# Kernel tuning notes

Hardware: AMD Instinct MI355X
Metric: run time of the kernel (lower is better)

Reference implementation:

```python
import jax, jax.numpy as jnp
import numpy as np

N = 50000      # nodes
E = 600000     # edges
C = 128        # in_channels
H = 128        # hidden_channels
O = 128        # out_channels
G = 512        # graphs in batch
BN_EPS = 1e-5


def setup_inputs() -> dict:
    key = jax.random.key(0)
    ks = jax.random.split(key, 16)

    def w(k, shape):
        return jax.random.normal(k, shape, dtype=jnp.float32) * 0.05

    inp = {}
    inp["x"] = jax.random.normal(ks[0], (N, C), dtype=jnp.float32)
    inp["edge_index"] = jax.random.randint(ks[1], (2, E), 0, N, dtype=jnp.int64)
    inp["batch"] = jnp.sort(jax.random.randint(ks[2], (N,), 0, G, dtype=jnp.int64))

    dims = [(C, H, H), (H, H, H), (H, H, O)]
    ki = 3
    for li, (din, dh, dout) in enumerate(dims, 1):
        inp[f"g{li}_W1"] = w(ks[ki], (din, dh)); inp[f"g{li}_b1"] = jnp.zeros((dh,), jnp.float32)
        inp[f"g{li}_gm"] = jnp.ones((dh,), jnp.float32); inp[f"g{li}_bt"] = jnp.zeros((dh,), jnp.float32)
        inp[f"g{li}_rm"] = jnp.zeros((dh,), jnp.float32); inp[f"g{li}_rv"] = jnp.ones((dh,), jnp.float32)
        inp[f"g{li}_W2"] = w(ks[ki + 1], (dh, dout)); inp[f"g{li}_b2"] = jnp.zeros((dout,), jnp.float32)
        ki += 2
    inp["lin_W"] = w(ks[ki], (H + H + O, O))
    inp["lin_b"] = jnp.zeros((O,), jnp.float32)
    return inp


def gin_conv(x, src, dst, W1, b1, gm, bt, rm, rv, W2, b2):
    # GINConv (eps=0): mlp(x + sum_{j in N(i)} x_j); mlp = Linear-BN(eval)-ReLU-Linear
    agg = jax.ops.segment_sum(x[src], dst, num_segments=N)   # [N, d] scatter-add
    h = (x + agg) @ W1 + b1
    h = (h - rm) * jax.lax.rsqrt(rv + BN_EPS) * gm + bt      # BatchNorm1d, eval mode
    return jax.nn.relu(h) @ W2 + b2


def reference(x, edge_index, batch,
              g1_W1, g1_b1, g1_gm, g1_bt, g1_rm, g1_rv, g1_W2, g1_b2,
              g2_W1, g2_b1, g2_gm, g2_bt, g2_rm, g2_rv, g2_W2, g2_b2,
              g3_W1, g3_b1, g3_gm, g3_bt, g3_rm, g3_rv, g3_W2, g3_b2,
              lin_W, lin_b):
    src, dst = edge_index[0], edge_index[1]
    # dropout(0.2) is identity in eval mode
    x1 = jax.nn.relu(gin_conv(x, src, dst, g1_W1, g1_b1, g1_gm, g1_bt, g1_rm, g1_rv, g1_W2, g1_b2))
    x2 = jax.nn.relu(gin_conv(x1, src, dst, g2_W1, g2_b1, g2_gm, g2_bt, g2_rm, g2_rv, g2_W2, g2_b2))
    x3 = gin_conv(x2, src, dst, g3_W1, g3_b1, g3_gm, g3_bt, g3_rm, g3_rv, g3_W2, g3_b2)
    xc = jnp.concatenate([x1, x2, x3], axis=-1)              # JumpingKnowledge 'cat' -> [N, H+H+O]
    sums = jax.ops.segment_sum(xc, batch, num_segments=G)    # global_mean_pool
    cnt = jax.ops.segment_sum(jnp.ones((N, 1), xc.dtype), batch, num_segments=G)
    pooled = sums / jnp.maximum(cnt, 1.0)                    # [G, H+H+O]
    return pooled @ lin_W + lin_b                            # [G, O]
```

## Files before the change

### kernel.cpp

```cpp
#include <hip/hip_runtime.h>
#include <hip/hip_bf16.h>

#define NNODES 50000
#define NEDGES 600000
#define NGRAPHS 512
#define BN_EPS 1e-5f

typedef short bf16x8 __attribute__((ext_vector_type(8)));
typedef float f32x4 __attribute__((ext_vector_type(4)));

__device__ __forceinline__ void bf_split(float x, ushort& h, ushort& l) {
    __hip_bfloat16 bh = __float2bfloat16(x);
    float r = x - __bfloat162float(bh);
    __hip_bfloat16 bl = __float2bfloat16(r);
    h = __builtin_bit_cast(ushort, bh);
    l = __builtin_bit_cast(ushort, bl);
}
__device__ __forceinline__ ushort f2b(float x) {
    return __builtin_bit_cast(ushort, __float2bfloat16(x));
}
__device__ __forceinline__ float b2f(ushort u) {
    union { uint i; float f; } c; c.i = ((uint)u) << 16; return c.f;
}

__global__ __launch_bounds__(256) void prep_kernel(
    const float* __restrict__ x, ushort* __restrict__ xh,
    float* __restrict__ pooled, const int* __restrict__ dst,
    int* __restrict__ counts, int* __restrict__ row_ptr,
    const float* W0, const float* W1, const float* W2, const float* W3,
    const float* W4, const float* W5, ushort* __restrict__ hi, ushort* __restrict__ lo) {
    int b = blockIdx.x, t = threadIdx.x;
    if (b < 3125) {
        int f4 = b * 512 + t * 2;
        float4 a0 = ((const float4*)x)[f4];
        float4 a1 = ((const float4*)x)[f4 + 1];
        ushort4 u0 = {f2b(a0.x), f2b(a0.y), f2b(a0.z), f2b(a0.w)};
        ushort4 u1 = {f2b(a1.x), f2b(a1.y), f2b(a1.z), f2b(a1.w)};
        int e0 = f4 * 4;
        *(ushort4*)(xh + e0) = u0;
        *(ushort4*)(xh + e0 + 4) = u1;
        if (b == 0 && t == 0) row_ptr[NNODES] = NEDGES;
    } else if (b < 3317) {
        ((float4*)pooled)[(b - 3125) * 256 + t] = make_float4(0.f, 0.f, 0.f, 0.f);
    } else if (b < 5661) {
        int i = (b - 3317) * 256 + t;
        if (i < NEDGES) atomicAdd(&counts[dst[i]], 1);
    } else {
        int wb = b - 5661;
        const float* Ws[6] = {W0, W1, W2, W3, W4, W5};
        const float* W = Ws[wb >> 4];
        ushort* h = hi + (size_t)(wb >> 4) * 16384;
        ushort* l = lo + (size_t)(wb >> 4) * 16384;
        int chunk = wb & 15;
#pragma unroll
        for (int i = 0; i < 4; i++) {
            int idx = chunk * 1024 + i * 256 + t;
            int j    = idx & 7;
            int lane = (idx >> 3) & 63;
            int nt   = (idx >> 9) & 7;
            int kb   = (idx >> 12) & 3;
            int k = kb * 32 + ((lane >> 4) << 3) + j;
            int n = nt * 16 + (lane & 15);
            ushort hh, ll;
            bf_split(W[k * 128 + n], hh, ll);
            h[idx] = hh;
            l[idx] = ll;
        }
    }
}

__global__ __launch_bounds__(256) void scan1_kernel(const int* __restrict__ counts,
                                                    int* __restrict__ partials, int n) {
    __shared__ int s[256];
    int i = blockIdx.x * 256 + threadIdx.x;
    int v = (i < n) ? counts[i] : 0;
    s[threadIdx.x] = v;
    __syncthreads();
    for (int off = 128; off > 0; off >>= 1) {
        if (threadIdx.x < off) s[threadIdx.x] += s[threadIdx.x + off];
        __syncthreads();
    }
    if (threadIdx.x == 0) partials[blockIdx.x] = s[0];
}

__global__ __launch_bounds__(256) void scan3_kernel(const int* __restrict__ counts,
                                                    const int* __restrict__ partials,
                                                    int* __restrict__ row_ptr,
                                                    int* __restrict__ cursor, int n, int nb) {
    __shared__ int s[256];
    __shared__ int base_sh;
    int t = threadIdx.x;
    int pv = (t < (int)blockIdx.x && t < nb) ? partials[t] : 0;
    s[t] = pv;
    __syncthreads();
    for (int off = 128; off > 0; off >>= 1) {
        if (t < off) s[t] += s[t + off];
        __syncthreads();
    }
    if (t == 0) base_sh = s[0];
    __syncthreads();
    int base = base_sh;
    int i = blockIdx.x * 256 + t;
    int v = (i < n) ? counts[i] : 0;
    __syncthreads();
    s[t] = v;
    __syncthreads();
    for (int off = 1; off < 256; off <<= 1) {
        int nv = (t >= off) ? s[t - off] : 0;
        __syncthreads();
        s[t] += nv;
        __syncthreads();
    }
    if (i < n) {
        int ex = base + s[t] - v;
        row_ptr[i] = ex;
        cursor[i] = ex;
    }
}

__global__ __launch_bounds__(256) void scatter_kernel(const int* __restrict__ src,
                                                      const int* __restrict__ dst,
                                                      int* __restrict__ cursor,
                                                      int* __restrict__ esrc, int E) {
    int i = blockIdx.x * 256 + threadIdx.x;
    if (i < E) {
        int p = atomicAdd(&cursor[dst[i]], 1);
        esrc[p] = src[i];
    }
}

__global__ __launch_bounds__(256) void agg_kernel(
    const ushort* __restrict__ phi,
    const int* __restrict__ rp, const int* __restrict__ esrc,
    ushort* __restrict__ ohi, int n) {
    int wid  = (blockIdx.x * 256 + threadIdx.x) >> 6;
    int lane = threadIdx.x & 63;
    int node = wid * 2 + (lane >> 5);
    int q = lane & 31;
    if (node >= n) return;
    const ushort4* xh = (const ushort4*)phi;
    ushort4 sh = xh[(size_t)node * 32 + q];
    float4 acc;
    acc.x = b2f(sh.x); acc.y = b2f(sh.y); acc.z = b2f(sh.z); acc.w = b2f(sh.w);
    int beg = rp[node], end = rp[node + 1];
    int e = beg;
    for (; e + 8 <= end; e += 8) {
        int i0 = esrc[e],     i1 = esrc[e + 1], i2 = esrc[e + 2], i3 = esrc[e + 3];
        int i4 = esrc[e + 4], i5 = esrc[e + 5], i6 = esrc[e + 6], i7 = esrc[e + 7];
        ushort4 v0 = xh[(size_t)i0 * 32 + q];
        ushort4 v1 = xh[(size_t)i1 * 32 + q];
        ushort4 v2 = xh[(size_t)i2 * 32 + q];
        ushort4 v3 = xh[(size_t)i3 * 32 + q];
        ushort4 v4 = xh[(size_t)i4 * 32 + q];
        ushort4 v5 = xh[(size_t)i5 * 32 + q];
        ushort4 v6 = xh[(size_t)i6 * 32 + q];
        ushort4 v7 = xh[(size_t)i7 * 32 + q];
        acc.x += ((b2f(v0.x) + b2f(v1.x)) + (b2f(v2.x) + b2f(v3.x))) +
                 ((b2f(v4.x) + b2f(v5.x)) + (b2f(v6.x) + b2f(v7.x)));
        acc.y += ((b2f(v0.y) + b2f(v1.y)) + (b2f(v2.y) + b2f(v3.y))) +
                 ((b2f(v4.y) + b2f(v5.y)) + (b2f(v6.y) + b2f(v7.y)));
        acc.z += ((b2f(v0.z) + b2f(v1.z)) + (b2f(v2.z) + b2f(v3.z))) +
                 ((b2f(v4.z) + b2f(v5.z)) + (b2f(v6.z) + b2f(v7.z)));
        acc.w += ((b2f(v0.w) + b2f(v1.w)) + (b2f(v2.w) + b2f(v3.w))) +
                 ((b2f(v4.w) + b2f(v5.w)) + (b2f(v6.w) + b2f(v7.w)));
    }
    for (; e + 2 <= end; e += 2) {
        int i0 = esrc[e], i1 = esrc[e + 1];
        ushort4 v0 = xh[(size_t)i0 * 32 + q];
        ushort4 v1 = xh[(size_t)i1 * 32 + q];
        acc.x += b2f(v0.x) + b2f(v1.x); acc.y += b2f(v0.y) + b2f(v1.y);
        acc.z += b2f(v0.z) + b2f(v1.z); acc.w += b2f(v0.w) + b2f(v1.w);
    }
    for (; e < end; e++) {
        ushort4 v = xh[(size_t)esrc[e] * 32 + q];
        acc.x += b2f(v.x); acc.y += b2f(v.y); acc.z += b2f(v.z); acc.w += b2f(v.w);
    }
    ushort4 hh = {f2b(acc.x), f2b(acc.y), f2b(acc.z), f2b(acc.w)};
    *(ushort4*)(ohi + (size_t)node * 128 + q * 4) = hh;
}

template <bool RELU_OUT, bool WRITE_PLANES>
__global__ __launch_bounds__(128) void mlp_kernel(
    const ushort* __restrict__ Ah,
    const ushort* __restrict__ W1hi, const ushort* __restrict__ W1lo,
    const ushort* __restrict__ W2hi, const ushort* __restrict__ W2lo,
    const float* __restrict__ b1, const float* __restrict__ gm,
    const float* __restrict__ bt, const float* __restrict__ rm,
    const float* __restrict__ rv, const float* __restrict__ b2,
    ushort* __restrict__ Ch,
    const int* __restrict__ batch, float* __restrict__ pooled, int poff, int M) {
    __shared__ __align__(16) ushort smem[64 * 136];
    __shared__ int bsm[64];
    const int t = threadIdx.x;
    const int lane = t & 63;
    const int wv = t >> 6;
    const int row0 = blockIdx.x * 64;
    const int g = lane >> 4, c = lane & 15;

    if (t < 64) bsm[t] = (row0 + t < M) ? batch[row0 + t] : -1;

    const int m0 = t >> 2, k80 = (t & 3) * 8;
    const int m1 = m0 + 32;
    int r0 = row0 + m0; if (r0 >= M) r0 = M - 1;
    int r1 = row0 + m1; if (r1 >= M) r1 = M - 1;
    const size_t ga0 = (size_t)r0 * 128 + k80;
    const size_t ga1 = (size_t)r1 * 128 + k80;
    const int la0 = m0 * 32 + k80, la1 = m1 * 32 + k80;

    f32x4 acc[4][4];
#pragma unroll
    for (int i = 0; i < 4; i++)
#pragma unroll
        for (int j = 0; j < 4; j++) acc[i][j] = (f32x4){0.f, 0.f, 0.f, 0.f};

    uint4 ph0 = *(const uint4*)(Ah + ga0);
    uint4 ph1 = *(const uint4*)(Ah + ga1);
    *(uint4*)&smem[la0] = ph0;
    *(uint4*)&smem[la1] = ph1;
    __syncthreads();

    int cur = 0;
    for (int kb = 0; kb < 4; kb++) {
        bf16x8 bh[4], bl[4];
#pragma unroll
        for (int ct = 0; ct < 4; ct++) {
            const size_t wo = (((size_t)kb * 8 + (wv * 4 + ct)) * 64 + lane) * 8;
            bh[ct] = *(const bf16x8*)(W1hi + wo);
            bl[ct] = *(const bf16x8*)(W1lo + wo);
        }
        if (kb < 3) {
            const size_t o = (size_t)(kb + 1) * 32;
            ph0 = *(const uint4*)(Ah + ga0 + o);
            ph1 = *(const uint4*)(Ah + ga1 + o);
        }
        bf16x8 ah[4];
#pragma unroll
        for (int rt = 0; rt < 4; rt++) {
            int off = cur * 4096 + (rt * 16 + c) * 32 + g * 8;
            ah[rt] = *(bf16x8*)&smem[off];
        }
#pragma unroll
        for (int rt = 0; rt < 4; rt++)
#pragma unroll
            for (int ct = 0; ct < 4; ct++) {
                acc[rt][ct] = __builtin_amdgcn_mfma_f32_16x16x32_bf16(ah[rt], bh[ct], acc[rt][ct], 0, 0, 0);
                acc[rt][ct] = __builtin_amdgcn_mfma_f32_16x16x32_bf16(ah[rt], bl[ct], acc[rt][ct], 0, 0, 0);
            }
        if (kb < 3) {
            *(uint4*)&smem[(cur ^ 1) * 4096 + la0] = ph0;
            *(uint4*)&smem[(cur ^ 1) * 4096 + la1] = ph1;
        }
        __syncthreads();
        cur ^= 1;
    }

    {
        float cs[4], ca[4];
#pragma unroll
        for (int ct = 0; ct < 4; ct++) {
            int n = wv * 64 + ct * 16 + c;
            float s = gm[n] * rsqrtf(rv[n] + BN_EPS);
            cs[ct] = s;
            ca[ct] = (b1[n] - rm[n]) * s + bt[n];
        }
#pragma unroll
        for (int rt = 0; rt < 4; rt++)
#pragma unroll
            for (int r = 0; r < 4; r++) {
                int row = rt * 16 + g * 4 + r;
#pragma unroll
                for (int ct = 0; ct < 4; ct++) {
                    int col = wv * 64 + ct * 16 + c;
                    float v = fmaxf(acc[rt][ct][r] * cs[ct] + ca[ct], 0.f);
                    smem[row * 136 + col] = f2b(v);
                }
            }
    }
    __syncthreads();

#pragma unroll
    for (int i = 0; i < 4; i++)
#pragma unroll
        for (int j = 0; j < 4; j++) acc[i][j] = (f32x4){0.f, 0.f, 0.f, 0.f};

    for (int kb = 0; kb < 4; kb++) {
        bf16x8 bh[4], bl[4];
#pragma unroll
        for (int ct = 0; ct < 4; ct++) {
            const size_t wo = (((size_t)kb * 8 + (wv * 4 + ct)) * 64 + lane) * 8;
            bh[ct] = *(const bf16x8*)(W2hi + wo);
            bl[ct] = *(const bf16x8*)(W2lo + wo);
        }
        bf16x8 ah[4];
#pragma unroll
        for (int rt = 0; rt < 4; rt++) {
            int off = (rt * 16 + c) * 136 + kb * 32 + g * 8;
            ah[rt] = *(bf16x8*)&smem[off];
        }
#pragma unroll
        for (int rt = 0; rt < 4; rt++)
#pragma unroll
            for (int ct = 0; ct < 4; ct++) {
                acc[rt][ct] = __builtin_amdgcn_mfma_f32_16x16x32_bf16(ah[rt], bh[ct], acc[rt][ct], 0, 0, 0);
                acc[rt][ct] = __builtin_amdgcn_mfma_f32_16x16x32_bf16(ah[rt], bl[ct], acc[rt][ct], 0, 0, 0);
            }
    }
    __syncthreads();

    {
        float ca2[4];
#pragma unroll
        for (int ct = 0; ct < 4; ct++) ca2[ct] = b2[wv * 64 + ct * 16 + c];
#pragma unroll
        for (int rt = 0; rt < 4; rt++)
#pragma unroll
            for (int r = 0; r < 4; r++) {
                int rl = rt * 16 + g * 4 + r;
                int row = row0 + rl;
                bool valid = row < M;
#pragma unroll
                for (int ct = 0; ct < 4; ct++) {
                    int col = wv * 64 + ct * 16 + c;
                    float v = acc[rt][ct][r] + ca2[ct];
                    if (RELU_OUT) v = fmaxf(v, 0.f);
                    ushort hh = f2b(valid ? v : 0.f);
                    smem[rl * 136 + col] = hh;
                    if (WRITE_PLANES && valid) Ch[(size_t)row * 128 + col] = hh;
                }
            }
    }
    __syncthreads();

    {
        int col = t;
        int gcur = bsm[0];
        float accp = 0.f;
#pragma unroll 8
        for (int r = 0; r < 64; r++) {
            int gg = bsm[r];
            if (gg != gcur) {
                if (gcur >= 0) atomicAdd(&pooled[gcur * 384 + poff + col], accp);
                accp = 0.f;
                gcur = gg;
            }
            accp += b2f(smem[r * 136 + col]);
        }
        if (gcur >= 0) atomicAdd(&pooled[gcur * 384 + poff + col], accp);
    }
}

__global__ __launch_bounds__(128) void final_kernel(const float* __restrict__ pooled,
                                                    const int* __restrict__ batch,
                                                    const float* __restrict__ W,
                                                    const float* __restrict__ b,
                                                    float* __restrict__ out, int n) {
    __shared__ float ps[384];
    int gph = blockIdx.x, t = threadIdx.x;
    int lo1 = 0, hi1 = n;
    while (lo1 < hi1) { int mid = (lo1 + hi1) >> 1; if (batch[mid] < gph) lo1 = mid + 1; else hi1 = mid; }
    int start = lo1;
    int lo2 = start, hi2 = n;
    while (lo2 < hi2) { int mid = (lo2 + hi2) >> 1; if (batch[mid] < gph + 1) lo2 = mid + 1; else hi2 = mid; }
    int cnt = lo2 - start;
    float inv = 1.f / (float)(cnt > 0 ? cnt : 1);
    for (int i = t; i < 384; i += 128) ps[i] = pooled[gph * 384 + i] * inv;
    __syncthreads();
    float acc = b[t];
#pragma unroll 8
    for (int k = 0; k < 384; k++) acc += ps[k] * W[k * 128 + t];
    out[gph * 128 + t] = acc;
}

extern "C" void kernel_launch(void* const* d_in, const int* in_sizes, int n_in,
                              void* d_out, int out_size, void* d_ws, size_t ws_size,
                              hipStream_t stream) {
    const float* x     = (const float*)d_in[0];
    const int*   edge  = (const int*)d_in[1];
    const int*   batch = (const int*)d_in[2];
    const float* p[32];
    for (int i = 0; i < n_in && i < 32; i++) p[i] = (const float*)d_in[i];
    const float* lin_W = p[27];
    const float* lin_b = p[28];

    char* w = (char*)d_ws;
    auto alloc = [&](size_t bytes) { void* r = (void*)w; w += (bytes + 255) & ~(size_t)255; return r; };
    const size_t PL = (size_t)NNODES * 128;
    ushort* thi   = (ushort*)alloc(PL * 2);
    ushort* xh0   = (ushort*)alloc(PL * 2);
    ushort* p1h   = (ushort*)alloc(PL * 2);
    ushort* p2h   = xh0;
    float* pooled = (float*)alloc((size_t)NGRAPHS * 384 * 4);
    int* counts   = (int*)alloc((size_t)NNODES * 4);
    int* cursor   = (int*)alloc((size_t)NNODES * 4);
    int* row_ptr  = (int*)alloc((size_t)(NNODES + 1) * 4);
    int* esrc     = (int*)alloc((size_t)NEDGES * 4);
    int* partials = (int*)alloc(256 * 4);
    ushort* wt_hi = (ushort*)alloc((size_t)6 * 16384 * 2);
    ushort* wt_lo = (ushort*)alloc((size_t)6 * 16384 * 2);

    const int* src = edge;
    const int* dst = edge + NEDGES;

    hipMemsetAsync(counts, 0, (size_t)NNODES * 4, stream);
    prep_kernel<<<5757, 256, 0, stream>>>(x, xh0, pooled, dst, counts, row_ptr,
                                          p[3], p[9], p[11], p[17], p[19], p[25],
                                          wt_hi, wt_lo);

    int nb = (NNODES + 255) / 256;
    scan1_kernel<<<nb, 256, 0, stream>>>(counts, partials, NNODES);
    scan3_kernel<<<nb, 256, 0, stream>>>(counts, partials, row_ptr, cursor, NNODES, nb);
    scatter_kernel<<<(NEDGES + 255) / 256, 256, 0, stream>>>(src, dst, cursor, esrc, NEDGES);

    int mlp_grid = (NNODES + 63) / 64;
    int agg_grid = (NNODES / 2 * 64 + 255) / 256;

    agg_kernel<<<agg_grid, 256, 0, stream>>>(xh0, row_ptr, esrc, thi, NNODES);
    mlp_kernel<true, true><<<mlp_grid, 128, 0, stream>>>(thi,
        wt_hi + 0 * 16384, wt_lo + 0 * 16384, wt_hi + 1 * 16384, wt_lo + 1 * 16384,
        p[4], p[5], p[6], p[7], p[8], p[10], p1h, batch, pooled, 0, NNODES);
    agg_kernel<<<agg_grid, 256, 0, stream>>>(p1h, row_ptr, esrc, thi, NNODES);
    mlp_kernel<true, true><<<mlp_grid, 128, 0, stream>>>(thi,
        wt_hi + 2 * 16384, wt_lo + 2 * 16384, wt_hi + 3 * 16384, wt_lo + 3 * 16384,
        p[12], p[13], p[14], p[15], p[16], p[18], p2h, batch, pooled, 128, NNODES);
    agg_kernel<<<agg_grid, 256, 0, stream>>>(p2h, row_ptr, esrc, thi, NNODES);
    mlp_kernel<false, false><<<mlp_grid, 128, 0, stream>>>(thi,
        wt_hi + 4 * 16384, wt_lo + 4 * 16384, wt_hi + 5 * 16384, wt_lo + 5 * 16384,
        p[20], p[21], p[22], p[23], p[24], p[26], nullptr, batch, pooled, 256, NNODES);

    final_kernel<<<NGRAPHS, 128, 0, stream>>>(pooled, batch, lin_W, lin_b,
                                              (float*)d_out, NNODES);
}
```

Measured before the change: 340.0 us.

## Fuse neighbor aggregation into the per-layer MLP kernel via shared memory

Merges the separate CSR gather-sum kernel into the MLP kernel. Each 64-row block first aggregates its own nodes' neighbor features, two nodes at a time per half-wave, and writes the bf16 result straight into a K-blocked shared-memory tile. This removes the intermediate aggregate buffer write and read and one launch per layer, and drops the double-buffered global A loads. The cost is that each block runs the irregular gather with only 128 threads, so there is less memory-level parallelism and more load imbalance before the MFMA phase can start.

```diff
diff --git a/kernel.cpp b/kernel.cpp
--- a/kernel.cpp
+++ b/kernel.cpp
@@ -129,59 +129,32 @@
     }
 }
 
-__global__ __launch_bounds__(256) void agg_kernel(
-    const ushort* __restrict__ phi,
+#define GB8(ACC, E0)                                                            \
+    {                                                                           \
+        int i0 = esrc[E0],     i1 = esrc[E0 + 1], i2 = esrc[E0 + 2], i3 = esrc[E0 + 3]; \
+        int i4 = esrc[E0 + 4], i5 = esrc[E0 + 5], i6 = esrc[E0 + 6], i7 = esrc[E0 + 7]; \
+        ushort4 v0 = xv[(size_t)i0 * 32 + q];                                   \
+        ushort4 v1 = xv[(size_t)i1 * 32 + q];                                   \
+        ushort4 v2 = xv[(size_t)i2 * 32 + q];                                   \
+        ushort4 v3 = xv[(size_t)i3 * 32 + q];                                   \
+        ushort4 v4 = xv[(size_t)i4 * 32 + q];                                   \
+        ushort4 v5 = xv[(size_t)i5 * 32 + q];                                   \
+        ushort4 v6 = xv[(size_t)i6 * 32 + q];                                   \
+        ushort4 v7 = xv[(size_t)i7 * 32 + q];                                   \
+        ACC.x += ((b2f(v0.x) + b2f(v1.x)) + (b2f(v2.x) + b2f(v3.x))) +          \
+                 ((b2f(v4.x) + b2f(v5.x)) + (b2f(v6.x) + b2f(v7.x)));           \
+        ACC.y += ((b2f(v0.y) + b2f(v1.y)) + (b2f(v2.y) + b2f(v3.y))) +          \
+                 ((b2f(v4.y) + b2f(v5.y)) + (b2f(v6.y) + b2f(v7.y)));           \
+        ACC.z += ((b2f(v0.z) + b2f(v1.z)) + (b2f(v2.z) + b2f(v3.z))) +          \
+                 ((b2f(v4.z) + b2f(v5.z)) + (b2f(v6.z) + b2f(v7.z)));           \
+        ACC.w += ((b2f(v0.w) + b2f(v1.w)) + (b2f(v2.w) + b2f(v3.w))) +          \
+                 ((b2f(v4.w) + b2f(v5.w)) + (b2f(v6.w) + b2f(v7.w)));           \
+    }
+
+template <bool RELU_OUT, bool WRITE_PLANES>
+__global__ __launch_bounds__(128) void layer_kernel(
+    const ushort* __restrict__ Pin,
     const int* __restrict__ rp, const int* __restrict__ esrc,
-    ushort* __restrict__ ohi, int n) {
-    int wid  = (blockIdx.x * 256 + threadIdx.x) >> 6;
-    int lane = threadIdx.x & 63;
-    int node = wid * 2 + (lane >> 5);
-    int q = lane & 31;
-    if (node >= n) return;
-    const ushort4* xh = (const ushort4*)phi;
-    ushort4 sh = xh[(size_t)node * 32 + q];
-    float4 acc;
-    acc.x = b2f(sh.x); acc.y = b2f(sh.y); acc.z = b2f(sh.z); acc.w = b2f(sh.w);
-    int beg = rp[node], end = rp[node + 1];
-    int e = beg;
-    for (; e + 8 <= end; e += 8) {
-        int i0 = esrc[e],     i1 = esrc[e + 1], i2 = esrc[e + 2], i3 = esrc[e + 3];
-        int i4 = esrc[e + 4], i5 = esrc[e + 5], i6 = esrc[e + 6], i7 = esrc[e + 7];
-        ushort4 v0 = xh[(size_t)i0 * 32 + q];
-        ushort4 v1 = xh[(size_t)i1 * 32 + q];
-        ushort4 v2 = xh[(size_t)i2 * 32 + q];
-        ushort4 v3 = xh[(size_t)i3 * 32 + q];
-        ushort4 v4 = xh[(size_t)i4 * 32 + q];
-        ushort4 v5 = xh[(size_t)i5 * 32 + q];
-        ushort4 v6 = xh[(size_t)i6 * 32 + q];
-        ushort4 v7 = xh[(size_t)i7 * 32 + q];
-        acc.x += ((b2f(v0.x) + b2f(v1.x)) + (b2f(v2.x) + b2f(v3.x))) +
-                 ((b2f(v4.x) + b2f(v5.x)) + (b2f(v6.x) + b2f(v7.x)));
-        acc.y += ((b2f(v0.y) + b2f(v1.y)) + (b2f(v2.y) + b2f(v3.y))) +
-                 ((b2f(v4.y) + b2f(v5.y)) + (b2f(v6.y) + b2f(v7.y)));
-        acc.z += ((b2f(v0.z) + b2f(v1.z)) + (b2f(v2.z) + b2f(v3.z))) +
-                 ((b2f(v4.z) + b2f(v5.z)) + (b2f(v6.z) + b2f(v7.z)));
-        acc.w += ((b2f(v0.w) + b2f(v1.w)) + (b2f(v2.w) + b2f(v3.w))) +
-                 ((b2f(v4.w) + b2f(v5.w)) + (b2f(v6.w) + b2f(v7.w)));
-    }
-    for (; e + 2 <= end; e += 2) {
-        int i0 = esrc[e], i1 = esrc[e + 1];
-        ushort4 v0 = xh[(size_t)i0 * 32 + q];
-        ushort4 v1 = xh[(size_t)i1 * 32 + q];
-        acc.x += b2f(v0.x) + b2f(v1.x); acc.y += b2f(v0.y) + b2f(v1.y);
-        acc.z += b2f(v0.z) + b2f(v1.z); acc.w += b2f(v0.w) + b2f(v1.w);
-    }
-    for (; e < end; e++) {
-        ushort4 v = xh[(size_t)esrc[e] * 32 + q];
-        acc.x += b2f(v.x); acc.y += b2f(v.y); acc.z += b2f(v.z); acc.w += b2f(v.w);
-    }
-    ushort4 hh = {f2b(acc.x), f2b(acc.y), f2b(acc.z), f2b(acc.w)};
-    *(ushort4*)(ohi + (size_t)node * 128 + q * 4) = hh;
-}
-
-template <bool RELU_OUT, bool WRITE_PLANES>
-__global__ __launch_bounds__(128) void mlp_kernel(
-    const ushort* __restrict__ Ah,
     const ushort* __restrict__ W1hi, const ushort* __restrict__ W1lo,
     const ushort* __restrict__ W2hi, const ushort* __restrict__ W2lo,
     const float* __restrict__ b1, const float* __restrict__ gm,
@@ -199,13 +172,88 @@
 
     if (t < 64) bsm[t] = (row0 + t < M) ? batch[row0 + t] : -1;
 
-    const int m0 = t >> 2, k80 = (t & 3) * 8;
-    const int m1 = m0 + 32;
-    int r0 = row0 + m0; if (r0 >= M) r0 = M - 1;
-    int r1 = row0 + m1; if (r1 >= M) r1 = M - 1;
-    const size_t ga0 = (size_t)r0 * 128 + k80;
-    const size_t ga1 = (size_t)r1 * 128 + k80;
-    const int la0 = m0 * 32 + k80, la1 = m1 * 32 + k80;
+    {
+        const int hw = t >> 5;
+        const int q  = t & 31;
+        const ushort4* xv = (const ushort4*)Pin;
+        for (int i = 0; i < 16; i += 2) {
+            const int mA = hw * 16 + i, mB = mA + 1;
+            const int nA = row0 + mA, nB = row0 + mB;
+            float4 aA = make_float4(0.f, 0.f, 0.f, 0.f);
+            float4 aB = make_float4(0.f, 0.f, 0.f, 0.f);
+            int eA = 0, endA = 0, eB = 0, endB = 0;
+            if (nA < M) {
+                ushort4 s = xv[(size_t)nA * 32 + q];
+                aA.x = b2f(s.x); aA.y = b2f(s.y); aA.z = b2f(s.z); aA.w = b2f(s.w);
+                eA = rp[nA]; endA = rp[nA + 1];
+            }
+            if (nB < M) {
+                ushort4 s = xv[(size_t)nB * 32 + q];
+                aB.x = b2f(s.x); aB.y = b2f(s.y); aB.z = b2f(s.z); aB.w = b2f(s.w);
+                eB = rp[nB]; endB = rp[nB + 1];
+            }
+            while (eA + 8 <= endA && eB + 8 <= endB) {
+                int a0 = esrc[eA],     a1 = esrc[eA + 1], a2 = esrc[eA + 2], a3 = esrc[eA + 3];
+                int a4 = esrc[eA + 4], a5 = esrc[eA + 5], a6 = esrc[eA + 6], a7 = esrc[eA + 7];
+                int b0 = esrc[eB],     b1_ = esrc[eB + 1], b2_ = esrc[eB + 2], b3 = esrc[eB + 3];
+                int b4 = esrc[eB + 4], b5 = esrc[eB + 5], b6 = esrc[eB + 6], b7 = esrc[eB + 7];
+                ushort4 uA0 = xv[(size_t)a0 * 32 + q], uA1 = xv[(size_t)a1 * 32 + q];
+                ushort4 uA2 = xv[(size_t)a2 * 32 + q], uA3 = xv[(size_t)a3 * 32 + q];
+                ushort4 uA4 = xv[(size_t)a4 * 32 + q], uA5 = xv[(size_t)a5 * 32 + q];
+                ushort4 uA6 = xv[(size_t)a6 * 32 + q], uA7 = xv[(size_t)a7 * 32 + q];
+                ushort4 uB0 = xv[(size_t)b0 * 32 + q], uB1 = xv[(size_t)b1_ * 32 + q];
+                ushort4 uB2 = xv[(size_t)b2_ * 32 + q], uB3 = xv[(size_t)b3 * 32 + q];
+                ushort4 uB4 = xv[(size_t)b4 * 32 + q], uB5 = xv[(size_t)b5 * 32 + q];
+                ushort4 uB6 = xv[(size_t)b6 * 32 + q], uB7 = xv[(size_t)b7 * 32 + q];
+                aA.x += ((b2f(uA0.x) + b2f(uA1.x)) + (b2f(uA2.x) + b2f(uA3.x))) +
+                        ((b2f(uA4.x) + b2f(uA5.x)) + (b2f(uA6.x) + b2f(uA7.x)));
+                aA.y += ((b2f(uA0.y) + b2f(uA1.y)) + (b2f(uA2.y) + b2f(uA3.y))) +
+                        ((b2f(uA4.y) + b2f(uA5.y)) + (b2f(uA6.y) + b2f(uA7.y)));
+                aA.z += ((b2f(uA0.z) + b2f(uA1.z)) + (b2f(uA2.z) + b2f(uA3.z))) +
+                        ((b2f(uA4.z) + b2f(uA5.z)) + (b2f(uA6.z) + b2f(uA7.z)));
+                aA.w += ((b2f(uA0.w) + b2f(uA1.w)) + (b2f(uA2.w) + b2f(uA3.w))) +
+                        ((b2f(uA4.w) + b2f(uA5.w)) + (b2f(uA6.w) + b2f(uA7.w)));
+                aB.x += ((b2f(uB0.x) + b2f(uB1.x)) + (b2f(uB2.x) + b2f(uB3.x))) +
+                        ((b2f(uB4.x) + b2f(uB5.x)) + (b2f(uB6.x) + b2f(uB7.x)));
+                aB.y += ((b2f(uB0.y) + b2f(uB1.y)) + (b2f(uB2.y) + b2f(uB3.y))) +
+                        ((b2f(uB4.y) + b2f(uB5.y)) + (b2f(uB6.y) + b2f(uB7.y)));
+                aB.z += ((b2f(uB0.z) + b2f(uB1.z)) + (b2f(uB2.z) + b2f(uB3.z))) +
+                        ((b2f(uB4.z) + b2f(uB5.z)) + (b2f(uB6.z) + b2f(uB7.z)));
+                aB.w += ((b2f(uB0.w) + b2f(uB1.w)) + (b2f(uB2.w) + b2f(uB3.w))) +
+                        ((b2f(uB4.w) + b2f(uB5.w)) + (b2f(uB6.w) + b2f(uB7.w)));
+                eA += 8; eB += 8;
+            }
+            for (; eA + 8 <= endA; eA += 8) GB8(aA, eA);
+            for (; eB + 8 <= endB; eB += 8) GB8(aB, eB);
+            for (; eA + 2 <= endA; eA += 2) {
+                int i0 = esrc[eA], i1 = esrc[eA + 1];
+                ushort4 v0 = xv[(size_t)i0 * 32 + q];
+                ushort4 v1 = xv[(size_t)i1 * 32 + q];
+                aA.x += b2f(v0.x) + b2f(v1.x); aA.y += b2f(v0.y) + b2f(v1.y);
+                aA.z += b2f(v0.z) + b2f(v1.z); aA.w += b2f(v0.w) + b2f(v1.w);
+            }
+            for (; eA < endA; eA++) {
+                ushort4 v = xv[(size_t)esrc[eA] * 32 + q];
+                aA.x += b2f(v.x); aA.y += b2f(v.y); aA.z += b2f(v.z); aA.w += b2f(v.w);
+            }
+            for (; eB + 2 <= endB; eB += 2) {
+                int i0 = esrc[eB], i1 = esrc[eB + 1];
+                ushort4 v0 = xv[(size_t)i0 * 32 + q];
+                ushort4 v1 = xv[(size_t)i1 * 32 + q];
+                aB.x += b2f(v0.x) + b2f(v1.x); aB.y += b2f(v0.y) + b2f(v1.y);
+                aB.z += b2f(v0.z) + b2f(v1.z); aB.w += b2f(v0.w) + b2f(v1.w);
+            }
+            for (; eB < endB; eB++) {
+                ushort4 v = xv[(size_t)esrc[eB] * 32 + q];
+                aB.x += b2f(v.x); aB.y += b2f(v.y); aB.z += b2f(v.z); aB.w += b2f(v.w);
+            }
+            ushort4 hA = {f2b(aA.x), f2b(aA.y), f2b(aA.z), f2b(aA.w)};
+            ushort4 hB = {f2b(aB.x), f2b(aB.y), f2b(aB.z), f2b(aB.w)};
+            *(ushort4*)&smem[(q >> 3) * 2048 + mA * 32 + (q & 7) * 4] = hA;
+            *(ushort4*)&smem[(q >> 3) * 2048 + mB * 32 + (q & 7) * 4] = hB;
+        }
+    }
+    __syncthreads();
 
     f32x4 acc[4][4];
 #pragma unroll
@@ -213,13 +261,6 @@
 #pragma unroll
         for (int j = 0; j < 4; j++) acc[i][j] = (f32x4){0.f, 0.f, 0.f, 0.f};
 
-    uint4 ph0 = *(const uint4*)(Ah + ga0);
-    uint4 ph1 = *(const uint4*)(Ah + ga1);
-    *(uint4*)&smem[la0] = ph0;
-    *(uint4*)&smem[la1] = ph1;
-    __syncthreads();
-
-    int cur = 0;
     for (int kb = 0; kb < 4; kb++) {
         bf16x8 bh[4], bl[4];
 #pragma unroll
@@ -228,15 +269,10 @@
             bh[ct] = *(const bf16x8*)(W1hi + wo);
             bl[ct] = *(const bf16x8*)(W1lo + wo);
         }
-        if (kb < 3) {
-            const size_t o = (size_t)(kb + 1) * 32;
-            ph0 = *(const uint4*)(Ah + ga0 + o);
-            ph1 = *(const uint4*)(Ah + ga1 + o);
-        }
         bf16x8 ah[4];
 #pragma unroll
         for (int rt = 0; rt < 4; rt++) {
-            int off = cur * 4096 + (rt * 16 + c) * 32 + g * 8;
+            int off = kb * 2048 + (rt * 16 + c) * 32 + g * 8;
             ah[rt] = *(bf16x8*)&smem[off];
         }
 #pragma unroll
@@ -246,13 +282,8 @@
                 acc[rt][ct] = __builtin_amdgcn_mfma_f32_16x16x32_bf16(ah[rt], bh[ct], acc[rt][ct], 0, 0, 0);
                 acc[rt][ct] = __builtin_amdgcn_mfma_f32_16x16x32_bf16(ah[rt], bl[ct], acc[rt][ct], 0, 0, 0);
             }
-        if (kb < 3) {
-            *(uint4*)&smem[(cur ^ 1) * 4096 + la0] = ph0;
-            *(uint4*)&smem[(cur ^ 1) * 4096 + la1] = ph1;
-        }
-        __syncthreads();
-        cur ^= 1;
-    }
+    }
+    __syncthreads();
 
     {
         float cs[4], ca[4];
@@ -385,7 +416,6 @@
     char* w = (char*)d_ws;
     auto alloc = [&](size_t bytes) { void* r = (void*)w; w += (bytes + 255) & ~(size_t)255; return r; };
     const size_t PL = (size_t)NNODES * 128;
-    ushort* thi   = (ushort*)alloc(PL * 2);
     ushort* xh0   = (ushort*)alloc(PL * 2);
     ushort* p1h   = (ushort*)alloc(PL * 2);
     ushort* p2h   = xh0;
@@ -411,19 +441,14 @@
     scan3_kernel<<<nb, 256, 0, stream>>>(counts, partials, row_ptr, cursor, NNODES, nb);
     scatter_kernel<<<(NEDGES + 255) / 256, 256, 0, stream>>>(src, dst, cursor, esrc, NEDGES);
 
-    int mlp_grid = (NNODES + 63) / 64;
-    int agg_grid = (NNODES / 2 * 64 + 255) / 256;
-
-    agg_kernel<<<agg_grid, 256, 0, stream>>>(xh0, row_ptr, esrc, thi, NNODES);
-    mlp_kernel<true, true><<<mlp_grid, 128, 0, stream>>>(thi,
+    int grid = (NNODES + 63) / 64;
+    layer_kernel<true, true><<<grid, 128, 0, stream>>>(xh0, row_ptr, esrc,
         wt_hi + 0 * 16384, wt_lo + 0 * 16384, wt_hi + 1 * 16384, wt_lo + 1 * 16384,
         p[4], p[5], p[6], p[7], p[8], p[10], p1h, batch, pooled, 0, NNODES);
-    agg_kernel<<<agg_grid, 256, 0, stream>>>(p1h, row_ptr, esrc, thi, NNODES);
-    mlp_kernel<true, true><<<mlp_grid, 128, 0, stream>>>(thi,
+    layer_kernel<true, true><<<grid, 128, 0, stream>>>(p1h, row_ptr, esrc,
         wt_hi + 2 * 16384, wt_lo + 2 * 16384, wt_hi + 3 * 16384, wt_lo + 3 * 16384,
         p[12], p[13], p[14], p[15], p[16], p[18], p2h, batch, pooled, 128, NNODES);
-    agg_kernel<<<agg_grid, 256, 0, stream>>>(p2h, row_ptr, esrc, thi, NNODES);
-    mlp_kernel<false, false><<<mlp_grid, 128, 0, stream>>>(thi,
+    layer_kernel<false, false><<<grid, 128, 0, stream>>>(p2h, row_ptr, esrc,
         wt_hi + 4 * 16384, wt_lo + 4 * 16384, wt_hi + 5 * 16384, wt_lo + 5 * 16384,
         p[20], p[21], p[22], p[23], p[24], p[26], nullptr, batch, pooled, 256, NNODES);
 
```

After: 411.5 us. 1.21x slower.
